# Optimization experiments

Hardware: AMD Instinct MI355X
Metric: run time of the kernel (lower is better)

The kernel has to match this reference:

```python
import jax, jax.numpy as jnp
import numpy as np

B = 524288   # Monte-Carlo sample batch
C = 64       # C1 hidden width
D = 4        # D1 hidden layers
L = 4        # positional encoding frequencies
CIN = (2 * L + 1) * 2 + 2  # cond (18) + z (2) = 20
EPS = 1e-12


def posenc(x):
    # x: (B,2) -> (B, 2*(2L+1)) : identity + sin/cos at 2^i frequencies
    feats = [x]
    for i in range(L):
        f = (2.0 ** i) * x
        feats.append(jnp.sin(f))
        feats.append(jnp.cos(f))
    return jnp.concatenate(feats, -1)


def mlp(x, W_in, b_in, W_hid, b_hid, W_out, b_out):
    h = jax.nn.silu(x @ W_in + b_in)
    for i in range(W_hid.shape[0]):  # small fixed layer count
        h = jax.nn.silu(h @ W_hid[i] + b_hid[i])
    return h @ W_out + b_out


def forward_wi(cond, z, W_in, b_in, W_hid, b_hid, W_out, b_out):
    Tz = mlp(jnp.concatenate([cond, z], -1), W_in, b_in, W_hid, b_hid, W_out, b_out)
    wi3 = jnp.concatenate([Tz[..., :2], jax.nn.softplus(Tz[..., 2:])], -1)
    norm = jnp.maximum(jnp.linalg.norm(wi3, axis=-1, keepdims=True), EPS)
    wi3 = wi3 / norm  # F.normalize
    return wi3[..., :2]


def setup_inputs() -> dict:
    key = jax.random.key(0)
    ks = jax.random.split(key, 8)
    wo = jax.random.uniform(ks[0], (B, 2), dtype=jnp.float32)
    z = jax.random.normal(ks[1], (B, 2), dtype=jnp.float32)
    W_in = jax.random.normal(ks[2], (CIN, C), dtype=jnp.float32) / np.sqrt(CIN)
    b_in = jnp.zeros((C,), jnp.float32)
    W_hid = jax.random.normal(ks[3], (D - 1, C, C), dtype=jnp.float32) / np.sqrt(C)
    b_hid = jnp.zeros((D - 1, C), jnp.float32)
    W_out = jax.random.normal(ks[4], (C, 3), dtype=jnp.float32) / np.sqrt(C)
    b_out = jnp.zeros((3,), jnp.float32)
    return dict(wo=wo, z=z, W_in=W_in, b_in=b_in, W_hid=W_hid, b_hid=b_hid,
                W_out=W_out, b_out=b_out)


def reference(wo, z, W_in, b_in, W_hid, b_hid, W_out, b_out):
    cond = posenc(wo)  # (B,18)
    f = lambda zz: forward_wi(cond, zz, W_in, b_in, W_hid, b_hid, W_out, b_out)
    # 2x2 Jacobian via two batched JVPs (columns of J)
    t0 = jnp.broadcast_to(jnp.array([1.0, 0.0], jnp.float32), z.shape)
    t1 = jnp.broadcast_to(jnp.array([0.0, 1.0], jnp.float32), z.shape)
    wi, d0 = jax.jvp(f, (z,), (t0,))  # d0 = dwi/dz0, (B,2)
    _, d1 = jax.jvp(f, (z,), (t1,))  # d1 = dwi/dz1, (B,2)
    detJ = d0[..., 0] * d1[..., 1] - d1[..., 0] * d0[..., 1]
    # pack (wi, detJ) as (B,3) for a single-array output
    return jnp.concatenate([wi, detJ[..., None]], -1)
```

## Files before the change

kernel.cpp:

```cpp
#include <hip/hip_runtime.h>
#include <math.h>


#define SAMP 64
#define NTHR 192
#define C 64
#define JR 48
#define JS (C - JR)

__device__ __forceinline__ float frcp(float x) { return __builtin_amdgcn_rcpf(x); }
__device__ __forceinline__ float fsig(float a) { return frcp(1.f + __expf(-a)); }
__device__ __forceinline__ float fsp(float a, float sg) {
    return sg * (1.f + a * (1.f - sg));
}

__global__ __launch_bounds__(NTHR, 4) void neu_kernel(
    const float* __restrict__ wo, const float* __restrict__ z,
    const float* __restrict__ W_in, const float* __restrict__ b_in,
    const float* __restrict__ W_hid, const float* __restrict__ b_hid,
    const float* __restrict__ W_out, const float* __restrict__ b_out,
    float* __restrict__ out)
{
    __shared__ float sh_a[C*SAMP];
    __shared__ float sh_sx[3][JS*SAMP];

    const int tid  = threadIdx.x;
    const int samp = tid & 63;
    const int wave = __builtin_amdgcn_readfirstlane(tid >> 6);
    const int gs   = blockIdx.x * SAMP + samp;

    float* sx = sh_sx[wave];

    float s[JR];
    float u[C];

    {
        float x[20];
        const float2 wv = *reinterpret_cast<const float2*>(wo + gs*2);
        x[0] = wv.x; x[1] = wv.y;
        float f0 = wv.x, f1 = wv.y;
        #pragma unroll
        for (int i = 0; i < 4; ++i) {
            x[2+4*i+0] = __sinf(f0);
            x[2+4*i+1] = __sinf(f1);
            x[2+4*i+2] = __cosf(f0);
            x[2+4*i+3] = __cosf(f1);
            f0 += f0; f1 += f1;
        }
        const float2 zv = *reinterpret_cast<const float2*>(z + gs*2);
        x[18] = zv.x;
        x[19] = zv.y;

        {
            const float* wr = W_in;
            #pragma unroll
            for (int j = 0; j < C; ++j) u[j] = fmaf(x[0], wr[j], b_in[j]);
        }
        #pragma unroll
        for (int k = 1; k < 20; ++k) {
            const float xk = x[k];
            const float* wr = W_in + k*C;
            #pragma unroll
            for (int j = 0; j < C; ++j) u[j] = fmaf(xk, wr[j], u[j]);
        }
        if (wave == 0) {
            #pragma unroll
            for (int j = 0; j < JR; ++j) { float a = u[j]; s[j] = a * fsig(a); }
            #pragma unroll
            for (int j = JR; j < C; ++j) { float a = u[j]; sx[(j-JR)*SAMP+samp] = a * fsig(a); }
        } else {
            const float* wr = W_in + (17 + wave)*C;
            #pragma unroll
            for (int j = 0; j < JR; ++j) {
                float a = u[j], sg = fsig(a);
                s[j] = fsp(a, sg) * wr[j];
            }
            #pragma unroll
            for (int j = JR; j < C; ++j) {
                float a = u[j], sg = fsig(a);
                sx[(j-JR)*SAMP+samp] = fsp(a, sg) * wr[j];
            }
        }
    }

    for (int l = 0; l < 3; ++l) {
        const float* Wl = W_hid + l*C*C;
        {
            const float m0 = s[0];
            const float* wr = Wl;
            #pragma unroll
            for (int j = 0; j < C; ++j) u[j] = m0 * wr[j];
        }
        #pragma unroll
        for (int k = 1; k < JR; ++k) {
            const float m = s[k];
            const float* wr = Wl + k*C;
            #pragma unroll
            for (int j = 0; j < C; ++j) u[j] = fmaf(m, wr[j], u[j]);
        }
        {
            float st[JS];
            #pragma unroll
            for (int i = 0; i < JS; ++i) st[i] = sx[i*SAMP + samp];
            #pragma unroll
            for (int k = JR; k < C; ++k) {
                const float m = st[k-JR];
                const float* wr = Wl + k*C;
                #pragma unroll
                for (int j = 0; j < C; ++j) u[j] = fmaf(m, wr[j], u[j]);
            }
        }
        if (wave == 0) {
            const float* bh = b_hid + l*C;
            #pragma unroll
            for (int j = 0; j < C; ++j) u[j] += bh[j];
            #pragma unroll
            for (int j = 0; j < C; ++j) sh_a[j*SAMP + samp] = u[j];
        }
        __syncthreads();
        if (wave == 0) {
            #pragma unroll
            for (int j = 0; j < JR; ++j) { float a = u[j]; s[j] = a * fsig(a); }
            #pragma unroll
            for (int j = JR; j < C; ++j) { float a = u[j]; sx[(j-JR)*SAMP+samp] = a * fsig(a); }
        } else {
            #pragma unroll
            for (int j = 0; j < JR; ++j) {
                float a = sh_a[j*SAMP + samp], sg = fsig(a);
                s[j] = fsp(a, sg) * u[j];
            }
            #pragma unroll
            for (int j = JR; j < C; ++j) {
                float a = sh_a[j*SAMP + samp], sg = fsig(a);
                sx[(j-JR)*SAMP+samp] = fsp(a, sg) * u[j];
            }
        }
        __syncthreads();
    }

    {
        float o0, o1, o2;
        if (wave == 0) { o0 = b_out[0]; o1 = b_out[1]; o2 = b_out[2]; }
        else           { o0 = 0.f;      o1 = 0.f;      o2 = 0.f;      }
        #pragma unroll
        for (int k = 0; k < JR; ++k) {
            o0 = fmaf(s[k], W_out[k*3+0], o0);
            o1 = fmaf(s[k], W_out[k*3+1], o1);
            o2 = fmaf(s[k], W_out[k*3+2], o2);
        }
        float st[JS];
        #pragma unroll
        for (int i = 0; i < JS; ++i) st[i] = sx[i*SAMP + samp];
        #pragma unroll
        for (int k = JR; k < C; ++k) {
            o0 = fmaf(st[k-JR], W_out[k*3+0], o0);
            o1 = fmaf(st[k-JR], W_out[k*3+1], o1);
            o2 = fmaf(st[k-JR], W_out[k*3+2], o2);
        }
        sh_a[(wave*3+0)*SAMP + samp] = o0;
        sh_a[(wave*3+1)*SAMP + samp] = o1;
        sh_a[(wave*3+2)*SAMP + samp] = o2;
    }
    __syncthreads();
    if (wave == 0) {
        float T0 = sh_a[0*SAMP+samp], T1 = sh_a[1*SAMP+samp], T2 = sh_a[2*SAMP+samp];
        float a0 = sh_a[3*SAMP+samp], a1 = sh_a[4*SAMP+samp], a2 = sh_a[5*SAMP+samp];
        float c0 = sh_a[6*SAMP+samp], c1 = sh_a[7*SAMP+samp], c2 = sh_a[8*SAMP+samp];
        float sg2 = 1.f / (1.f + expf(-T2));
        float u2  = fmaxf(T2, 0.f) + log1pf(expf(-fabsf(T2)));
        float u0 = T0, u1 = T1;
        float n2  = u0*u0 + u1*u1 + u2*u2;
        float n   = fmaxf(sqrtf(n2), 1e-12f);
        float inv = 1.f / n;
        float da2 = sg2 * a2, dc2 = sg2 * c2;
        float ka  = (u0*a0 + u1*a1 + u2*da2) / n2;
        float kc  = (u0*c0 + u1*c1 + u2*dc2) / n2;
        float d0x = (a0 - u0*ka) * inv;
        float d0y = (a1 - u1*ka) * inv;
        float d1x = (c0 - u0*kc) * inv;
        float d1y = (c1 - u1*kc) * inv;
        float detJ = d0x*d1y - d1x*d0y;
        out[gs*3+0] = u0 * inv;
        out[gs*3+1] = u1 * inv;
        out[gs*3+2] = detJ;
    }
}

extern "C" void kernel_launch(void* const* d_in, const int* in_sizes, int n_in,
                              void* d_out, int out_size, void* d_ws, size_t ws_size,
                              hipStream_t stream) {
    const float* wo    = (const float*)d_in[0];
    const float* zz    = (const float*)d_in[1];
    const float* W_in  = (const float*)d_in[2];
    const float* b_in  = (const float*)d_in[3];
    const float* W_hid = (const float*)d_in[4];
    const float* b_hid = (const float*)d_in[5];
    const float* W_out = (const float*)d_in[6];
    const float* b_out = (const float*)d_in[7];
    float* o = (float*)d_out;

    const int B = in_sizes[0] / 2;
    const int nblk = B / SAMP;
    neu_kernel<<<nblk, NTHR, 0, stream>>>(wo, zz, W_in, b_in, W_hid, b_hid,
                                          W_out, b_out, o);
}
```

Measured before the change: 623.3 us.

## Switch MLP matmuls to packed fp16 dot2 with pre-packed weights

Adds a small pre-pass kernel that packs W_in, W_hid and W_out into fp16 pairs along the reduction dimension. The main kernel then accumulates with v_dot2 (fp16 inputs, fp32 accumulation), which halves the FMA instruction count. Activations and tangents are also kept as packed half2 in registers, so the LDS spill arrays used before are no longer needed. The cost is reduced precision on inputs, weights and tangents, which could hurt accuracy of the Jacobian determinant, plus one extra kernel launch per call.

```diff
diff --git a/kernel.cpp b/kernel.cpp
--- a/kernel.cpp
+++ b/kernel.cpp
@@ -5,34 +5,65 @@
 #define SAMP 64
 #define NTHR 192
 #define C 64
-#define JR 48
-#define JS (C - JR)
+
+typedef __fp16 half2_t __attribute__((ext_vector_type(2)));
 
 __device__ __forceinline__ float frcp(float x) { return __builtin_amdgcn_rcpf(x); }
 __device__ __forceinline__ float fsig(float a) { return frcp(1.f + __expf(-a)); }
 __device__ __forceinline__ float fsp(float a, float sg) {
     return sg * (1.f + a * (1.f - sg));
 }
+__device__ __forceinline__ half2_t pk(float lo, float hi) {
+    return __builtin_amdgcn_cvt_pkrtz(lo, hi);
+}
+__device__ __forceinline__ float fdot2(half2_t a, half2_t b, float c) {
+#if __has_builtin(__builtin_amdgcn_fdot2)
+    return __builtin_amdgcn_fdot2(a, b, c, false);
+#else
+    return fmaf((float)a.x, (float)b.x, fmaf((float)a.y, (float)b.y, c));
+#endif
+}
+
+#define WP_HID 640
+#define WP_OUT 6784
+#define WP_TOT 6880
+
+__global__ void pack_kernel(const float* __restrict__ W_in,
+                            const float* __restrict__ W_hid,
+                            const float* __restrict__ W_out,
+                            half2_t* __restrict__ wp)
+{
+    int i = blockIdx.x * 256 + threadIdx.x;
+    if (i < WP_HID) {
+        int p = i >> 6, j = i & 63;
+        wp[i] = pk(W_in[(2*p)*C + j], W_in[(2*p+1)*C + j]);
+    } else if (i < WP_OUT) {
+        int t = i - WP_HID;
+        int l = t >> 11, r = t & 2047, p = r >> 6, j = r & 63;
+        wp[i] = pk(W_hid[l*C*C + (2*p)*C + j], W_hid[l*C*C + (2*p+1)*C + j]);
+    } else if (i < WP_TOT) {
+        int t = i - WP_OUT;
+        int p = t / 3, q = t - p*3;
+        wp[i] = pk(W_out[(2*p)*3 + q], W_out[(2*p+1)*3 + q]);
+    }
+}
 
 __global__ __launch_bounds__(NTHR, 4) void neu_kernel(
     const float* __restrict__ wo, const float* __restrict__ z,
     const float* __restrict__ W_in, const float* __restrict__ b_in,
-    const float* __restrict__ W_hid, const float* __restrict__ b_hid,
-    const float* __restrict__ W_out, const float* __restrict__ b_out,
+    const float* __restrict__ b_hid, const float* __restrict__ b_out,
+    const half2_t* __restrict__ wp,
     float* __restrict__ out)
 {
     __shared__ float sh_a[C*SAMP];
-    __shared__ float sh_sx[3][JS*SAMP];
 
     const int tid  = threadIdx.x;
     const int samp = tid & 63;
     const int wave = __builtin_amdgcn_readfirstlane(tid >> 6);
     const int gs   = blockIdx.x * SAMP + samp;
 
-    float* sx = sh_sx[wave];
-
-    float s[JR];
-    float u[C];
+    float   u[C];
+    half2_t spk[32];
 
     {
         float x[20];
@@ -51,64 +82,52 @@
         x[18] = zv.x;
         x[19] = zv.y;
 
+        half2_t xp[10];
+        #pragma unroll
+        for (int p = 0; p < 10; ++p) xp[p] = pk(x[2*p], x[2*p+1]);
+
         {
-            const float* wr = W_in;
-            #pragma unroll
-            for (int j = 0; j < C; ++j) u[j] = fmaf(x[0], wr[j], b_in[j]);
-        }
-        #pragma unroll
-        for (int k = 1; k < 20; ++k) {
-            const float xk = x[k];
-            const float* wr = W_in + k*C;
-            #pragma unroll
-            for (int j = 0; j < C; ++j) u[j] = fmaf(xk, wr[j], u[j]);
+            const half2_t* wr = wp;
+            #pragma unroll
+            for (int j = 0; j < C; ++j) u[j] = fdot2(xp[0], wr[j], b_in[j]);
+        }
+        #pragma unroll
+        for (int p = 1; p < 10; ++p) {
+            const half2_t* wr = wp + p*C;
+            #pragma unroll
+            for (int j = 0; j < C; ++j) u[j] = fdot2(xp[p], wr[j], u[j]);
         }
         if (wave == 0) {
             #pragma unroll
-            for (int j = 0; j < JR; ++j) { float a = u[j]; s[j] = a * fsig(a); }
-            #pragma unroll
-            for (int j = JR; j < C; ++j) { float a = u[j]; sx[(j-JR)*SAMP+samp] = a * fsig(a); }
+            for (int p = 0; p < 32; ++p) {
+                float a0 = u[2*p],   h0 = a0 * fsig(a0);
+                float a1 = u[2*p+1], h1 = a1 * fsig(a1);
+                spk[p] = pk(h0, h1);
+            }
         } else {
             const float* wr = W_in + (17 + wave)*C;
             #pragma unroll
-            for (int j = 0; j < JR; ++j) {
-                float a = u[j], sg = fsig(a);
-                s[j] = fsp(a, sg) * wr[j];
-            }
-            #pragma unroll
-            for (int j = JR; j < C; ++j) {
-                float a = u[j], sg = fsig(a);
-                sx[(j-JR)*SAMP+samp] = fsp(a, sg) * wr[j];
+            for (int p = 0; p < 32; ++p) {
+                float a0 = u[2*p],   t0 = fsp(a0, fsig(a0)) * wr[2*p];
+                float a1 = u[2*p+1], t1 = fsp(a1, fsig(a1)) * wr[2*p+1];
+                spk[p] = pk(t0, t1);
             }
         }
     }
 
     for (int l = 0; l < 3; ++l) {
-        const float* Wl = W_hid + l*C*C;
+        const half2_t* Wl = wp + WP_HID + l*32*C;
         {
-            const float m0 = s[0];
-            const float* wr = Wl;
-            #pragma unroll
-            for (int j = 0; j < C; ++j) u[j] = m0 * wr[j];
-        }
-        #pragma unroll
-        for (int k = 1; k < JR; ++k) {
-            const float m = s[k];
-            const float* wr = Wl + k*C;
-            #pragma unroll
-            for (int j = 0; j < C; ++j) u[j] = fmaf(m, wr[j], u[j]);
-        }
-        {
-            float st[JS];
-            #pragma unroll
-            for (int i = 0; i < JS; ++i) st[i] = sx[i*SAMP + samp];
-            #pragma unroll
-            for (int k = JR; k < C; ++k) {
-                const float m = st[k-JR];
-                const float* wr = Wl + k*C;
-                #pragma unroll
-                for (int j = 0; j < C; ++j) u[j] = fmaf(m, wr[j], u[j]);
-            }
+            const half2_t m0 = spk[0];
+            #pragma unroll
+            for (int j = 0; j < C; ++j) u[j] = fdot2(m0, Wl[j], 0.f);
+        }
+        #pragma unroll
+        for (int p = 1; p < 32; ++p) {
+            const half2_t m = spk[p];
+            const half2_t* wr = Wl + p*C;
+            #pragma unroll
+            for (int j = 0; j < C; ++j) u[j] = fdot2(m, wr[j], u[j]);
         }
         if (wave == 0) {
             const float* bh = b_hid + l*C;
@@ -120,19 +139,19 @@
         __syncthreads();
         if (wave == 0) {
             #pragma unroll
-            for (int j = 0; j < JR; ++j) { float a = u[j]; s[j] = a * fsig(a); }
-            #pragma unroll
-            for (int j = JR; j < C; ++j) { float a = u[j]; sx[(j-JR)*SAMP+samp] = a * fsig(a); }
+            for (int p = 0; p < 32; ++p) {
+                float a0 = u[2*p],   h0 = a0 * fsig(a0);
+                float a1 = u[2*p+1], h1 = a1 * fsig(a1);
+                spk[p] = pk(h0, h1);
+            }
         } else {
             #pragma unroll
-            for (int j = 0; j < JR; ++j) {
-                float a = sh_a[j*SAMP + samp], sg = fsig(a);
-                s[j] = fsp(a, sg) * u[j];
-            }
-            #pragma unroll
-            for (int j = JR; j < C; ++j) {
-                float a = sh_a[j*SAMP + samp], sg = fsig(a);
-                sx[(j-JR)*SAMP+samp] = fsp(a, sg) * u[j];
+            for (int p = 0; p < 32; ++p) {
+                float a0 = sh_a[(2*p)*SAMP + samp];
+                float a1 = sh_a[(2*p+1)*SAMP + samp];
+                float t0 = fsp(a0, fsig(a0)) * u[2*p];
+                float t1 = fsp(a1, fsig(a1)) * u[2*p+1];
+                spk[p] = pk(t0, t1);
             }
         }
         __syncthreads();
@@ -142,20 +161,12 @@
         float o0, o1, o2;
         if (wave == 0) { o0 = b_out[0]; o1 = b_out[1]; o2 = b_out[2]; }
         else           { o0 = 0.f;      o1 = 0.f;      o2 = 0.f;      }
-        #pragma unroll
-        for (int k = 0; k < JR; ++k) {
-            o0 = fmaf(s[k], W_out[k*3+0], o0);
-            o1 = fmaf(s[k], W_out[k*3+1], o1);
-            o2 = fmaf(s[k], W_out[k*3+2], o2);
-        }
-        float st[JS];
-        #pragma unroll
-        for (int i = 0; i < JS; ++i) st[i] = sx[i*SAMP + samp];
-        #pragma unroll
-        for (int k = JR; k < C; ++k) {
-            o0 = fmaf(st[k-JR], W_out[k*3+0], o0);
-            o1 = fmaf(st[k-JR], W_out[k*3+1], o1);
-            o2 = fmaf(st[k-JR], W_out[k*3+2], o2);
+        const half2_t* wr = wp + WP_OUT;
+        #pragma unroll
+        for (int p = 0; p < 32; ++p) {
+            o0 = fdot2(spk[p], wr[p*3+0], o0);
+            o1 = fdot2(spk[p], wr[p*3+1], o1);
+            o2 = fdot2(spk[p], wr[p*3+2], o2);
         }
         sh_a[(wave*3+0)*SAMP + samp] = o0;
         sh_a[(wave*3+1)*SAMP + samp] = o1;
@@ -198,9 +209,12 @@
     const float* W_out = (const float*)d_in[6];
     const float* b_out = (const float*)d_in[7];
     float* o = (float*)d_out;
+    half2_t* wp = (half2_t*)d_ws;
+
+    pack_kernel<<<(WP_TOT + 255)/256, 256, 0, stream>>>(W_in, W_hid, W_out, wp);
 
     const int B = in_sizes[0] / 2;
     const int nblk = B / SAMP;
-    neu_kernel<<<nblk, NTHR, 0, stream>>>(wo, zz, W_in, b_in, W_hid, b_hid,
-                                          W_out, b_out, o);
-}
+    neu_kernel<<<nblk, NTHR, 0, stream>>>(wo, zz, W_in, b_in, b_hid, b_out,
+                                          wp, o);
+}
```

After: 582.7 us. -6.5%, faster.
